# Optimization experiments

Measured on AMD Instinct MI355X. Metric: run time of the kernel, lower is better.

The kernel has to match this reference:

```python
import jax, jax.numpy as jnp
import numpy as np

D_MODEL = 1024
N_HEAD = 16
D_K = D_MODEL // N_HEAD


def setup_inputs() -> dict:
    key = jax.random.key(0)
    ks = jax.random.split(key, 11)
    B, S = 2, 2048
    std = 1.0 / np.sqrt(D_MODEL)
    inp = {
        "Q": jax.random.normal(ks[0], (B, S, D_MODEL), jnp.float32),
        "K": jax.random.normal(ks[1], (B, S, D_MODEL), jnp.float32),
        "V": jax.random.normal(ks[2], (B, S, D_MODEL), jnp.float32),
        "Wq": jax.random.normal(ks[3], (D_MODEL, D_MODEL), jnp.float32) * std,
        "bq": jnp.zeros((D_MODEL,), jnp.float32),
        "Wk": jax.random.normal(ks[4], (D_MODEL, D_MODEL), jnp.float32) * std,
        "bk": jnp.zeros((D_MODEL,), jnp.float32),
        "Wv": jax.random.normal(ks[5], (D_MODEL, D_MODEL), jnp.float32) * std,
        "bv": jnp.zeros((D_MODEL,), jnp.float32),
        "Wo": jax.random.normal(ks[6], (D_MODEL, D_MODEL), jnp.float32) * std,
        "bo": jnp.zeros((D_MODEL,), jnp.float32),
    }
    return inp


def _split_heads(x):
    # [B, S, D] -> [B, H, S, d_k]
    B, S, _ = x.shape
    return x.reshape(B, S, N_HEAD, D_K).transpose(0, 2, 1, 3)


def reference(Q, K, V, Wq, bq, Wk, bk, Wv, bv, Wo, bo):
    q = _split_heads(Q @ Wq.T + bq)   # [B,H,S,dk]
    k = _split_heads(K @ Wk.T + bk)
    v = _split_heads(V @ Wv.T + bv)
    scale = 1.0 / jnp.sqrt(jnp.float32(D_K))
    scores = jnp.einsum("bhqd,bhkd->bhqk", q, k) * scale
    attn = jax.nn.softmax(scores, axis=-1)
    ctx = jnp.einsum("bhqk,bhkd->bhqd", attn, v)  # [B,H,S,dk]
    B, H, S, dk = ctx.shape
    ctx = ctx.transpose(0, 2, 1, 3).reshape(B, S, H * dk)
    return ctx @ Wo.T + bo
```

## Files before the change

kernel.cpp:

```cpp
#include <hip/hip_runtime.h>
#include <hip/hip_bf16.h>
#include <cstdint>
#include <cstddef>
#include <cmath>

typedef __attribute__((ext_vector_type(8))) short short8;
typedef __attribute__((ext_vector_type(4))) short short4_t;
typedef __attribute__((ext_vector_type(4))) float f32x4;
typedef __attribute__((ext_vector_type(16))) float f32x16;

constexpr int B_ = 2, S_ = 2048, H_ = 16, DK_ = 64, DM_ = 1024;

__device__ inline unsigned short f2bf(float x) {
  union { float f; unsigned u; } c; c.f = x;
  unsigned r = c.u + 0x7FFF + ((c.u >> 16) & 1);
  return (unsigned short)(r >> 16);
}

__device__ inline float ex2(float x) {
#if __has_builtin(__builtin_amdgcn_exp2f)
  return __builtin_amdgcn_exp2f(x);
#else
  return exp2f(x);
#endif
}

__device__ inline unsigned pkbf(float lo, float hi) {
  unsigned u;
  asm("v_cvt_pk_bf16_f32 %0, %1, %2" : "=v"(u) : "v"(lo), "v"(hi));
  return u;
}

__device__ inline f32x4 mfma16(short8 a, short8 b, f32x4 c) {
  return __builtin_amdgcn_mfma_f32_16x16x32_bf16(a, b, c, 0, 0, 0);
}
__device__ inline f32x16 mfma32(short8 a, short8 b, f32x16 c) {
  return __builtin_amdgcn_mfma_f32_32x32x16_bf16(a, b, c, 0, 0, 0);
}

__device__ inline void glds16(const unsigned short* g, unsigned short* l) {
  __builtin_amdgcn_global_load_lds(
      (const __attribute__((address_space(1))) unsigned int*)g,
      (__attribute__((address_space(3))) unsigned int*)l, 16, 0, 0);
}

__global__ __launch_bounds__(256) void cvt_all(
    const float* __restrict__ Q, const float* __restrict__ K,
    const float* __restrict__ V, const float* __restrict__ Wq,
    const float* __restrict__ Wk, const float* __restrict__ Wv,
    const float* __restrict__ Wo, unsigned short* __restrict__ Qb,
    unsigned short* __restrict__ Kb, unsigned short* __restrict__ Vb,
    unsigned short* __restrict__ Wqb, unsigned short* __restrict__ Wkb,
    unsigned short* __restrict__ Wvb, unsigned short* __restrict__ Wob) {
  int bid = blockIdx.x;
  const float* in; unsigned short* out; int off;
  if (bid < 4096)       { in = Q;  out = Qb;  off = bid; }
  else if (bid < 8192)  { in = K;  out = Kb;  off = bid - 4096; }
  else if (bid < 12288) { in = V;  out = Vb;  off = bid - 8192; }
  else if (bid < 13312) { in = Wq; out = Wqb; off = bid - 12288; }
  else if (bid < 14336) { in = Wk; out = Wkb; off = bid - 13312; }
  else if (bid < 15360) { in = Wv; out = Wvb; off = bid - 14336; }
  else                  { in = Wo; out = Wob; off = bid - 15360; }
  int i = off * 256 + threadIdx.x;
  float4 f = ((const float4*)in)[i];
  uint2 o;
  o.x = pkbf(f.x, f.y);
  o.y = pkbf(f.z, f.w);
  ((uint2*)out)[i] = o;
}

__device__ inline void store_out(float* p, float v) { *p = v; }
__device__ inline void store_out(unsigned short* p, float v) { *p = f2bf(v); }

template <typename OUT_T>
__device__ inline void gemm_body(const unsigned short* __restrict__ A,
                                 const unsigned short* __restrict__ Bw,
                                 const float* __restrict__ bias,
                                 OUT_T* __restrict__ C, float cscale,
                                 int bm, int bn) {
  constexpr int Kd = 1024, Nd = 1024, NSTEP = Kd / 64;
  __shared__ unsigned short As[2][128][64];
  __shared__ unsigned short Bs[2][64][64];

  const int tid = threadIdx.x;
  const int lane = tid & 63, wave = tid >> 6;
  const int li = lane & 15, lg = lane >> 4;
  const int wm = wave >> 1, wn = wave & 1;

  const f32x4 zero4 = {0.f, 0.f, 0.f, 0.f};
  f32x4 acc[4][2];
#pragma unroll
  for (int i = 0; i < 4; i++)
#pragma unroll
    for (int j = 0; j < 2; j++) acc[i][j] = zero4;

  const int stg_row = tid >> 3;
  const int stg_col = (tid & 7) * 8;
  const unsigned short* Ag = A + (size_t)(bm * 128 + stg_row) * Kd + stg_col;
  const unsigned short* Bg = Bw + (size_t)(bn * 64 + stg_row) * Kd + stg_col;

#pragma unroll
  for (int i = 0; i < 4; i++)
    glds16(Ag + (size_t)(i * 32) * Kd, &As[0][i * 32 + stg_row][stg_col]);
#pragma unroll
  for (int i = 0; i < 2; i++)
    glds16(Bg + (size_t)(i * 32) * Kd, &Bs[0][i * 32 + stg_row][stg_col]);

  for (int kt = 0; kt < NSTEP; kt++) {
    const int buf = kt & 1;
    asm volatile("s_waitcnt vmcnt(0)" ::: "memory");
    __builtin_amdgcn_sched_barrier(0);
    __builtin_amdgcn_s_barrier();
    __builtin_amdgcn_sched_barrier(0);

    if (kt + 1 < NSTEP) {
      const int kof = (kt + 1) * 64;
#pragma unroll
      for (int i = 0; i < 4; i++)
        glds16(Ag + (size_t)(i * 32) * Kd + kof,
               &As[buf ^ 1][i * 32 + stg_row][stg_col]);
#pragma unroll
      for (int i = 0; i < 2; i++)
        glds16(Bg + (size_t)(i * 32) * Kd + kof,
               &Bs[buf ^ 1][i * 32 + stg_row][stg_col]);
    }
    __builtin_amdgcn_sched_barrier(0);

    short8 af[4][2], bf[2][2];
#pragma unroll
    for (int kb = 0; kb < 2; kb++) {
#pragma unroll
      for (int i = 0; i < 4; i++)
        af[i][kb] =
            *(const short8*)&As[buf][wm * 64 + i * 16 + li][kb * 32 + lg * 8];
#pragma unroll
      for (int j = 0; j < 2; j++)
        bf[j][kb] =
            *(const short8*)&Bs[buf][wn * 32 + j * 16 + li][kb * 32 + lg * 8];
    }
#pragma unroll
    for (int kb = 0; kb < 2; kb++)
#pragma unroll
      for (int i = 0; i < 4; i++)
#pragma unroll
        for (int j = 0; j < 2; j++)
          acc[i][j] = mfma16(af[i][kb], bf[j][kb], acc[i][j]);
  }

#pragma unroll
  for (int j = 0; j < 2; j++) {
    int col = bn * 64 + wn * 32 + j * 16 + li;
    float bv = bias[col];
#pragma unroll
    for (int i = 0; i < 4; i++) {
      int row0 = bm * 128 + wm * 64 + i * 16 + lg * 4;
#pragma unroll
      for (int r = 0; r < 4; r++)
        store_out(&C[(size_t)(row0 + r) * Nd + col], (acc[i][j][r] + bv) * cscale);
    }
  }
}

__global__ __launch_bounds__(256, 3) void gemm_qkv(
    const unsigned short* __restrict__ Aq, const unsigned short* __restrict__ Ak,
    const unsigned short* __restrict__ Av, const unsigned short* __restrict__ Bq,
    const unsigned short* __restrict__ Bk, const unsigned short* __restrict__ Bv,
    const float* __restrict__ bq, const float* __restrict__ bk,
    const float* __restrict__ bv, unsigned short* __restrict__ Cq,
    unsigned short* __restrict__ Ck, unsigned short* __restrict__ Cv,
    float qscale) {
  const int n = blockIdx.x;
  const int xcd = n & 7, m = n >> 3;
  const int z = m >> 6, idx = m & 63;
  const int bm = xcd * 4 + (idx >> 4), bn = idx & 15;
  const unsigned short* A = z == 0 ? Aq : z == 1 ? Ak : Av;
  const unsigned short* Bw = z == 0 ? Bq : z == 1 ? Bk : Bv;
  const float* bi = z == 0 ? bq : z == 1 ? bk : bv;
  unsigned short* C = z == 0 ? Cq : z == 1 ? Ck : Cv;
  gemm_body(A, Bw, bi, C, z == 0 ? qscale : 1.0f, bm, bn);
}

__global__ __launch_bounds__(256, 3) void gemm_out(
    const unsigned short* __restrict__ A, const unsigned short* __restrict__ Bw,
    const float* __restrict__ bias, float* __restrict__ C) {
  const int n = blockIdx.x;
  const int xcd = n & 7, m = n >> 3;
  const int bm = xcd * 4 + (m >> 4), bn = m & 15;
  gemm_body(A, Bw, bias, C, 1.0f, bm, bn);
}

struct V4 { short8 v[4]; };

__device__ __forceinline__ void attn_tile_step(
    int kt, int buf, int NT,
    const unsigned short* kg, const unsigned short* vg,
    unsigned short* KsAll, unsigned short* VtAll,
    int srow, int sc, int scs, int key2, int dq,
    const short8* qf, int l31, int h,
    V4& vc, V4& vn, f32x16* po, float& m_i, float& l_i) {
  unsigned short* KsB = KsAll + buf * (128 * 64);
  unsigned short* VtB = VtAll + buf * (64 * 128);
  unsigned short* KsO = KsAll + (buf ^ 1) * (128 * 64);

  asm volatile("s_waitcnt vmcnt(0)" ::: "memory");
  __builtin_amdgcn_sched_barrier(0);

#pragma unroll
  for (int j = 0; j < 16; j++) {
    const int half = j >> 3, jj = j & 7;
    unsigned w = (unsigned)(unsigned short)vc.v[half][jj] |
                 ((unsigned)(unsigned short)vc.v[2 + half][jj] << 16);
    const int slot = (key2 >> 3) ^ j;
    *(unsigned*)&VtB[(dq * 16 + j) * 128 + slot * 8 + (key2 & 7)] = w;
  }

  if (kt + 1 < NT) {
    const unsigned short* vp =
        vg + (size_t)((kt + 1) * 128 + key2) * DM_ + dq * 16;
    vn.v[0] = *(const short8*)(vp);
    vn.v[1] = *(const short8*)(vp + 8);
    vn.v[2] = *(const short8*)(vp + DM_);
    vn.v[3] = *(const short8*)(vp + DM_ + 8);
  }

  asm volatile("s_waitcnt lgkmcnt(0)" ::: "memory");
  __builtin_amdgcn_sched_barrier(0);
  __builtin_amdgcn_s_barrier();
  __builtin_amdgcn_sched_barrier(0);

  if (kt + 1 < NT) {
    const unsigned short* kgt = kg + (size_t)((kt + 1) * 128) * DM_;
#pragma unroll
    for (int i = 0; i < 4; i++)
      glds16(kgt + (size_t)(i * 32 + srow) * DM_ + scs,
             &KsO[(i * 32 + srow) * 64 + sc * 8]);
  }
  __builtin_amdgcn_sched_barrier(0);

  f32x16 sacc[4];
#pragma unroll
  for (int kb = 0; kb < 4; kb++)
#pragma unroll
    for (int r = 0; r < 16; r++) sacc[kb][r] = 0.f;

  __builtin_amdgcn_s_setprio(1);
#pragma unroll
  for (int tq = 0; tq < 4; tq++) {
    const int sl = ((((tq << 1) | h) ^ (l31 & 7))) * 8;
#pragma unroll
    for (int kb = 0; kb < 4; kb++) {
      short8 kf = *(const short8*)&KsB[(kb * 32 + l31) * 64 + sl];
      sacc[kb] = mfma32(kf, qf[tq], sacc[kb]);
    }
  }
  __builtin_amdgcn_s_setprio(0);

  float mx = -1e30f;
#pragma unroll
  for (int kb = 0; kb < 4; kb++)
#pragma unroll
    for (int r = 0; r < 16; r += 4)
      mx = fmaxf(mx, fmaxf(fmaxf(sacc[kb][r], sacc[kb][r + 1]),
                           fmaxf(sacc[kb][r + 2], sacc[kb][r + 3])));
  mx = fmaxf(mx, __shfl_xor(mx, 32));

  if (!__all(mx - m_i <= 8.0f)) {
    float mn = fmaxf(m_i, mx);
    float al = ex2(m_i - mn);
    m_i = mn;
    l_i *= al;
#pragma unroll
    for (int db = 0; db < 2; db++)
#pragma unroll
      for (int r = 0; r < 16; r++) po[db][r] *= al;
  }

  float s0 = 0.f, s1 = 0.f, s2 = 0.f, s3 = 0.f;
#pragma unroll
  for (int kb = 0; kb < 4; kb++) {
#pragma unroll
    for (int r = 0; r < 16; r += 4) {
      float p0 = ex2(sacc[kb][r] - m_i);
      float p1 = ex2(sacc[kb][r + 1] - m_i);
      float p2 = ex2(sacc[kb][r + 2] - m_i);
      float p3 = ex2(sacc[kb][r + 3] - m_i);
      sacc[kb][r] = p0; sacc[kb][r + 1] = p1;
      sacc[kb][r + 2] = p2; sacc[kb][r + 3] = p3;
      s0 += p0; s1 += p1; s2 += p2; s3 += p3;
    }
    unsigned u[4][2];
#pragma unroll
    for (int qd = 0; qd < 4; qd++) {
      u[qd][0] = pkbf(sacc[kb][4 * qd], sacc[kb][4 * qd + 1]);
      u[qd][1] = pkbf(sacc[kb][4 * qd + 2], sacc[kb][4 * qd + 3]);
    }
    __builtin_amdgcn_s_setprio(1);
#pragma unroll
    for (int tt = 0; tt < 2; tt++) {
      const int tp = 2 * kb + tt, qe = tt * 2;
      unsigned X0 = u[qe][0], X1 = u[qe][1];
      unsigned Y0 = u[qe + 1][0], Y1 = u[qe + 1][1];
      unsigned sX0 = __shfl_xor(X0, 32), sX1 = __shfl_xor(X1, 32);
      unsigned sY0 = __shfl_xor(Y0, 32), sY1 = __shfl_xor(Y1, 32);
      union { unsigned w[4]; short8 v8; } fr;
      fr.w[0] = h ? sY0 : X0;
      fr.w[1] = h ? sY1 : X1;
      fr.w[2] = h ? Y0 : sX0;
      fr.w[3] = h ? Y1 : sX1;
      const int slbase = (tp << 1) | h;
#pragma unroll
      for (int db = 0; db < 2; db++) {
        const int row = db * 32 + l31;
        short8 vf = *(const short8*)
            &VtB[row * 128 + (slbase ^ (l31 & 15)) * 8];
        po[db] = mfma32(vf, fr.v8, po[db]);
      }
    }
    __builtin_amdgcn_s_setprio(0);
  }
  float sum = (s0 + s1) + (s2 + s3);
  sum += __shfl_xor(sum, 32);
  l_i += sum;
}

__global__ __launch_bounds__(256, 2) void attn_fwd(
    const unsigned short* __restrict__ q, const unsigned short* __restrict__ k,
    const unsigned short* __restrict__ v, unsigned short* __restrict__ ctx) {
  __shared__ unsigned short Ks[2][128][64];
  __shared__ unsigned short Vt[2][64][128];

  const int tid = threadIdx.x;
  const int lane = tid & 63, wave = tid >> 6;
  const int l31 = lane & 31, h = lane >> 5;
  const int n = blockIdx.x;
  const int xcd = n & 7, m = n >> 3;
  const int bh = xcd * 4 + (m & 3);
  const int qt = m >> 2;
  const int b = bh >> 4, hd = bh & 15;

  const int qrow = qt * 128 + wave * 32 + l31;
  const unsigned short* qg = q + (size_t)(b * S_ + qrow) * DM_ + hd * DK_;
  short8 qf[4];
#pragma unroll
  for (int t = 0; t < 4; t++) qf[t] = *(const short8*)(qg + t * 16 + h * 8);

  f32x16 po[2];
#pragma unroll
  for (int db = 0; db < 2; db++)
#pragma unroll
    for (int r = 0; r < 16; r++) po[db][r] = 0.f;
  float m_i = -1e30f, l_i = 0.f;

  const int srow = tid >> 3, sc = tid & 7;
  const int scs = (sc ^ (srow & 7)) * 8;
  const unsigned short* kg = k + (size_t)(b * S_) * DM_ + hd * DK_;

  const int key2 = (tid & 63) * 2, dq = tid >> 6;
  const unsigned short* vg = v + (size_t)(b * S_) * DM_ + hd * DK_;

  const int NT = S_ / 128;

#pragma unroll
  for (int i = 0; i < 4; i++)
    glds16(kg + (size_t)(i * 32 + srow) * DM_ + scs,
           &Ks[0][i * 32 + srow][sc * 8]);
  V4 va, vb;
  {
    const unsigned short* vp = vg + (size_t)key2 * DM_ + dq * 16;
    va.v[0] = *(const short8*)(vp);
    va.v[1] = *(const short8*)(vp + 8);
    va.v[2] = *(const short8*)(vp + DM_);
    va.v[3] = *(const short8*)(vp + DM_ + 8);
  }

  unsigned short* KsAll = &Ks[0][0][0];
  unsigned short* VtAll = &Vt[0][0][0];
  for (int it = 0; it < NT; it += 2) {
    attn_tile_step(it, 0, NT, kg, vg, KsAll, VtAll, srow, sc, scs, key2, dq,
                   qf, l31, h, va, vb, po, m_i, l_i);
    attn_tile_step(it + 1, 1, NT, kg, vg, KsAll, VtAll, srow, sc, scs, key2,
                   dq, qf, l31, h, vb, va, po, m_i, l_i);
  }

  float rl = 1.0f / l_i;
  unsigned short* cg = ctx + (size_t)(b * S_ + qrow) * DM_ + hd * DK_;
#pragma unroll
  for (int db = 0; db < 2; db++)
#pragma unroll
    for (int rq = 0; rq < 4; rq++) {
      uint2 w2;
      w2.x = pkbf(po[db][4 * rq] * rl, po[db][4 * rq + 1] * rl);
      w2.y = pkbf(po[db][4 * rq + 2] * rl, po[db][4 * rq + 3] * rl);
      *(uint2*)(cg + db * 32 + 8 * rq + 4 * h) = w2;
    }
}

extern "C" void kernel_launch(void* const* d_in, const int* in_sizes, int n_in,
                              void* d_out, int out_size, void* d_ws, size_t ws_size,
                              hipStream_t stream) {
  const float* Q  = (const float*)d_in[0];
  const float* Kx = (const float*)d_in[1];
  const float* V  = (const float*)d_in[2];
  const float* Wq = (const float*)d_in[3];
  const float* bq = (const float*)d_in[4];
  const float* Wk = (const float*)d_in[5];
  const float* bk = (const float*)d_in[6];
  const float* Wv = (const float*)d_in[7];
  const float* bv = (const float*)d_in[8];
  const float* Wo = (const float*)d_in[9];
  const float* bo = (const float*)d_in[10];
  float* out = (float*)d_out;

  char* ws = (char*)d_ws;
  const size_t MB = 1ull << 20;
  unsigned short* Qb  = (unsigned short*)(ws + 0 * MB);
  unsigned short* Kb  = (unsigned short*)(ws + 8 * MB);
  unsigned short* Vb  = (unsigned short*)(ws + 16 * MB);
  unsigned short* Wqb = (unsigned short*)(ws + 24 * MB);
  unsigned short* Wkb = (unsigned short*)(ws + 26 * MB);
  unsigned short* Wvb = (unsigned short*)(ws + 28 * MB);
  unsigned short* Wob = (unsigned short*)(ws + 30 * MB);
  unsigned short* qp  = (unsigned short*)(ws + 32 * MB);
  unsigned short* kp  = (unsigned short*)(ws + 40 * MB);
  unsigned short* vp  = (unsigned short*)(ws + 48 * MB);
  unsigned short* cx  = (unsigned short*)(ws + 56 * MB);

  cvt_all<<<16384, 256, 0, stream>>>(Q, Kx, V, Wq, Wk, Wv, Wo,
                                     Qb, Kb, Vb, Wqb, Wkb, Wvb, Wob);

  gemm_qkv<<<1536, 256, 0, stream>>>(
      Qb, Kb, Vb, Wqb, Wkb, Wvb, bq, bk, bv, qp, kp, vp, 0.18033688f);

  attn_fwd<<<512, 256, 0, stream>>>(qp, kp, vp, cx);

  gemm_out<<<512, 256, 0, stream>>>(cx, Wob, bo, out);
}
```

Measured before the change: 138.5 us.

## Use single-buffered 128x128 tiles for QKV GEMM and drop XCD block remapping

The QKV projection GEMM now uses 128x128 output tiles with a single LDS buffer and __syncthreads, instead of double-buffered 128x64 tiles. Its grid becomes a 3D dim3(32,8,3) launch. Both GEMMs drop the XCD-aware block index swizzle and use plain blockIdx mapping, and the output GEMM gets its own specialized float body. Larger tiles give more data reuse per loaded element and fewer blocks. The cost is losing load/compute overlap, losing L2 locality per XCD, and possibly lower occupancy since the launch bounds minimum was removed.

```diff
diff --git a/kernel.cpp b/kernel.cpp
--- a/kernel.cpp
+++ b/kernel.cpp
@@ -73,14 +73,14 @@
 __device__ inline void store_out(unsigned short* p, float v) { *p = f2bf(v); }
 
 template <typename OUT_T>
-__device__ inline void gemm_body(const unsigned short* __restrict__ A,
-                                 const unsigned short* __restrict__ Bw,
-                                 const float* __restrict__ bias,
-                                 OUT_T* __restrict__ C, float cscale,
-                                 int bm, int bn) {
-  constexpr int Kd = 1024, Nd = 1024, NSTEP = Kd / 64;
-  __shared__ unsigned short As[2][128][64];
-  __shared__ unsigned short Bs[2][64][64];
+__device__ inline void gemm128_body(const unsigned short* __restrict__ A,
+                                    const unsigned short* __restrict__ Bw,
+                                    const float* __restrict__ bias,
+                                    OUT_T* __restrict__ C, float cscale,
+                                    int bm, int bn) {
+  constexpr int Kd = 1024, Nd = 1024;
+  __shared__ unsigned short As[128][64];
+  __shared__ unsigned short Bs[128][64];
 
   const int tid = threadIdx.x;
   const int lane = tid & 63, wave = tid >> 6;
@@ -88,68 +88,46 @@
   const int wm = wave >> 1, wn = wave & 1;
 
   const f32x4 zero4 = {0.f, 0.f, 0.f, 0.f};
-  f32x4 acc[4][2];
+  f32x4 acc[4][4];
 #pragma unroll
   for (int i = 0; i < 4; i++)
 #pragma unroll
-    for (int j = 0; j < 2; j++) acc[i][j] = zero4;
-
-  const int stg_row = tid >> 3;
-  const int stg_col = (tid & 7) * 8;
-  const unsigned short* Ag = A + (size_t)(bm * 128 + stg_row) * Kd + stg_col;
-  const unsigned short* Bg = Bw + (size_t)(bn * 64 + stg_row) * Kd + stg_col;
-
-#pragma unroll
-  for (int i = 0; i < 4; i++)
-    glds16(Ag + (size_t)(i * 32) * Kd, &As[0][i * 32 + stg_row][stg_col]);
-#pragma unroll
-  for (int i = 0; i < 2; i++)
-    glds16(Bg + (size_t)(i * 32) * Kd, &Bs[0][i * 32 + stg_row][stg_col]);
-
-  for (int kt = 0; kt < NSTEP; kt++) {
-    const int buf = kt & 1;
-    asm volatile("s_waitcnt vmcnt(0)" ::: "memory");
-    __builtin_amdgcn_sched_barrier(0);
-    __builtin_amdgcn_s_barrier();
-    __builtin_amdgcn_sched_barrier(0);
-
-    if (kt + 1 < NSTEP) {
-      const int kof = (kt + 1) * 64;
+    for (int j = 0; j < 4; j++) acc[i][j] = zero4;
+
+  const int srow = tid >> 3;
+  const int scol = (tid & 7) * 8;
+  const unsigned short* Ag = A + (size_t)(bm * 128 + srow) * Kd + scol;
+  const unsigned short* Bg = Bw + (size_t)(bn * 128 + srow) * Kd + scol;
+
+  for (int kt = 0; kt < Kd; kt += 64) {
+#pragma unroll
+    for (int i = 0; i < 4; i++) {
+      glds16(Ag + (size_t)(i * 32) * Kd + kt, &As[i * 32 + srow][scol]);
+      glds16(Bg + (size_t)(i * 32) * Kd + kt, &Bs[i * 32 + srow][scol]);
+    }
+    __syncthreads();
+
+    short8 af[4][2], bf[4][2];
+#pragma unroll
+    for (int kb = 0; kb < 2; kb++)
+#pragma unroll
+      for (int i = 0; i < 4; i++) {
+        af[i][kb] = *(const short8*)&As[wm * 64 + i * 16 + li][kb * 32 + lg * 8];
+        bf[i][kb] = *(const short8*)&Bs[wn * 64 + i * 16 + li][kb * 32 + lg * 8];
+      }
+#pragma unroll
+    for (int kb = 0; kb < 2; kb++)
 #pragma unroll
       for (int i = 0; i < 4; i++)
-        glds16(Ag + (size_t)(i * 32) * Kd + kof,
-               &As[buf ^ 1][i * 32 + stg_row][stg_col]);
-#pragma unroll
-      for (int i = 0; i < 2; i++)
-        glds16(Bg + (size_t)(i * 32) * Kd + kof,
-               &Bs[buf ^ 1][i * 32 + stg_row][stg_col]);
-    }
-    __builtin_amdgcn_sched_barrier(0);
-
-    short8 af[4][2], bf[2][2];
-#pragma unroll
-    for (int kb = 0; kb < 2; kb++) {
-#pragma unroll
-      for (int i = 0; i < 4; i++)
-        af[i][kb] =
-            *(const short8*)&As[buf][wm * 64 + i * 16 + li][kb * 32 + lg * 8];
-#pragma unroll
-      for (int j = 0; j < 2; j++)
-        bf[j][kb] =
-            *(const short8*)&Bs[buf][wn * 32 + j * 16 + li][kb * 32 + lg * 8];
-    }
-#pragma unroll
-    for (int kb = 0; kb < 2; kb++)
-#pragma unroll
-      for (int i = 0; i < 4; i++)
-#pragma unroll
-        for (int j = 0; j < 2; j++)
+#pragma unroll
+        for (int j = 0; j < 4; j++)
           acc[i][j] = mfma16(af[i][kb], bf[j][kb], acc[i][j]);
-  }
-
-#pragma unroll
-  for (int j = 0; j < 2; j++) {
-    int col = bn * 64 + wn * 32 + j * 16 + li;
+    __syncthreads();
+  }
+
+#pragma unroll
+  for (int j = 0; j < 4; j++) {
+    int col = bn * 128 + wn * 64 + j * 16 + li;
     float bv = bias[col];
 #pragma unroll
     for (int i = 0; i < 4; i++) {
@@ -161,7 +139,7 @@
   }
 }
 
-__global__ __launch_bounds__(256, 3) void gemm_qkv(
+__global__ __launch_bounds__(256) void gemm_qkv(
     const unsigned short* __restrict__ Aq, const unsigned short* __restrict__ Ak,
     const unsigned short* __restrict__ Av, const unsigned short* __restrict__ Bq,
     const unsigned short* __restrict__ Bk, const unsigned short* __restrict__ Bv,
@@ -169,24 +147,105 @@
     const float* __restrict__ bv, unsigned short* __restrict__ Cq,
     unsigned short* __restrict__ Ck, unsigned short* __restrict__ Cv,
     float qscale) {
-  const int n = blockIdx.x;
-  const int xcd = n & 7, m = n >> 3;
-  const int z = m >> 6, idx = m & 63;
-  const int bm = xcd * 4 + (idx >> 4), bn = idx & 15;
+  const int z = blockIdx.z;
   const unsigned short* A = z == 0 ? Aq : z == 1 ? Ak : Av;
   const unsigned short* Bw = z == 0 ? Bq : z == 1 ? Bk : Bv;
   const float* bi = z == 0 ? bq : z == 1 ? bk : bv;
   unsigned short* C = z == 0 ? Cq : z == 1 ? Ck : Cv;
-  gemm_body(A, Bw, bi, C, z == 0 ? qscale : 1.0f, bm, bn);
+  gemm128_body(A, Bw, bi, C, z == 0 ? qscale : 1.0f, blockIdx.x, blockIdx.y);
+}
+
+__device__ inline void gemm_body(const unsigned short* __restrict__ A,
+                                 const unsigned short* __restrict__ Bw,
+                                 const float* __restrict__ bias,
+                                 float* __restrict__ C, int bm, int bn) {
+  constexpr int Kd = 1024, Nd = 1024, NSTEP = Kd / 64;
+  __shared__ unsigned short As[2][128][64];
+  __shared__ unsigned short Bs[2][64][64];
+
+  const int tid = threadIdx.x;
+  const int lane = tid & 63, wave = tid >> 6;
+  const int li = lane & 15, lg = lane >> 4;
+  const int wm = wave >> 1, wn = wave & 1;
+
+  const f32x4 zero4 = {0.f, 0.f, 0.f, 0.f};
+  f32x4 acc[4][2];
+#pragma unroll
+  for (int i = 0; i < 4; i++)
+#pragma unroll
+    for (int j = 0; j < 2; j++) acc[i][j] = zero4;
+
+  const int stg_row = tid >> 3;
+  const int stg_col = (tid & 7) * 8;
+  const unsigned short* Ag = A + (size_t)(bm * 128 + stg_row) * Kd + stg_col;
+  const unsigned short* Bg = Bw + (size_t)(bn * 64 + stg_row) * Kd + stg_col;
+
+#pragma unroll
+  for (int i = 0; i < 4; i++)
+    glds16(Ag + (size_t)(i * 32) * Kd, &As[0][i * 32 + stg_row][stg_col]);
+#pragma unroll
+  for (int i = 0; i < 2; i++)
+    glds16(Bg + (size_t)(i * 32) * Kd, &Bs[0][i * 32 + stg_row][stg_col]);
+
+  for (int kt = 0; kt < NSTEP; kt++) {
+    const int buf = kt & 1;
+    asm volatile("s_waitcnt vmcnt(0)" ::: "memory");
+    __builtin_amdgcn_sched_barrier(0);
+    __builtin_amdgcn_s_barrier();
+    __builtin_amdgcn_sched_barrier(0);
+
+    if (kt + 1 < NSTEP) {
+      const int kof = (kt + 1) * 64;
+#pragma unroll
+      for (int i = 0; i < 4; i++)
+        glds16(Ag + (size_t)(i * 32) * Kd + kof,
+               &As[buf ^ 1][i * 32 + stg_row][stg_col]);
+#pragma unroll
+      for (int i = 0; i < 2; i++)
+        glds16(Bg + (size_t)(i * 32) * Kd + kof,
+               &Bs[buf ^ 1][i * 32 + stg_row][stg_col]);
+    }
+    __builtin_amdgcn_sched_barrier(0);
+
+    short8 af[4][2], bf[2][2];
+#pragma unroll
+    for (int kb = 0; kb < 2; kb++) {
+#pragma unroll
+      for (int i = 0; i < 4; i++)
+        af[i][kb] =
+            *(const short8*)&As[buf][wm * 64 + i * 16 + li][kb * 32 + lg * 8];
+#pragma unroll
+      for (int j = 0; j < 2; j++)
+        bf[j][kb] =
+            *(const short8*)&Bs[buf][wn * 32 + j * 16 + li][kb * 32 + lg * 8];
+    }
+#pragma unroll
+    for (int kb = 0; kb < 2; kb++)
+#pragma unroll
+      for (int i = 0; i < 4; i++)
+#pragma unroll
+        for (int j = 0; j < 2; j++)
+          acc[i][j] = mfma16(af[i][kb], bf[j][kb], acc[i][j]);
+  }
+
+#pragma unroll
+  for (int j = 0; j < 2; j++) {
+    int col = bn * 64 + wn * 32 + j * 16 + li;
+    float bv = bias[col];
+#pragma unroll
+    for (int i = 0; i < 4; i++) {
+      int row0 = bm * 128 + wm * 64 + i * 16 + lg * 4;
+#pragma unroll
+      for (int r = 0; r < 4; r++)
+        store_out(&C[(size_t)(row0 + r) * Nd + col], acc[i][j][r] + bv);
+    }
+  }
 }
 
 __global__ __launch_bounds__(256, 3) void gemm_out(
     const unsigned short* __restrict__ A, const unsigned short* __restrict__ Bw,
     const float* __restrict__ bias, float* __restrict__ C) {
-  const int n = blockIdx.x;
-  const int xcd = n & 7, m = n >> 3;
-  const int bm = xcd * 4 + (m >> 4), bn = m & 15;
-  gemm_body(A, Bw, bias, C, 1.0f, bm, bn);
+  gemm_body(A, Bw, bias, C, blockIdx.x, blockIdx.y);
 }
 
 struct V4 { short8 v[4]; };
@@ -428,10 +487,10 @@
   cvt_all<<<16384, 256, 0, stream>>>(Q, Kx, V, Wq, Wk, Wv, Wo,
                                      Qb, Kb, Vb, Wqb, Wkb, Wvb, Wob);
 
-  gemm_qkv<<<1536, 256, 0, stream>>>(
+  gemm_qkv<<<dim3(32, 8, 3), 256, 0, stream>>>(
       Qb, Kb, Vb, Wqb, Wkb, Wvb, bq, bk, bv, qp, kp, vp, 0.18033688f);
 
   attn_fwd<<<512, 256, 0, stream>>>(qp, kp, vp, cx);
 
-  gemm_out<<<512, 256, 0, stream>>>(cx, Wob, bo, out);
-}
+  gemm_out<<<dim3(32, 16), 256, 0, stream>>>(cx, Wob, bo, out);
+}
```

Result: no change. 139.6 us (+0.7%).
